# Kernel optimization log

Hardware: AMD Instinct MI355X
Metric: run time of the kernel (lower is better)

Reference implementation:

```python
import jax, jax.numpy as jnp
import numpy as np

N, E = 50000, 800000
IN_DIM, OUT_DIM, EDGE_DIM = 128, 128, 6
LN_EPS = 1e-5


def setup_inputs() -> dict:
    key = jax.random.key(0)
    ks = jax.random.split(key, 9)
    w = lambda k, sh: (jax.random.normal(k, sh, jnp.float32) * 0.05)
    return {
        "x": jax.random.normal(ks[0], (N, IN_DIM), jnp.float32),
        "edge_attr": jax.random.normal(ks[1], (E, EDGE_DIM), jnp.float32),
        "Wn": w(ks[2], (IN_DIM, OUT_DIM)),
        "bn": jnp.zeros((OUT_DIM,), jnp.float32),
        "We": w(ks[3], (EDGE_DIM, OUT_DIM)),
        "be": jnp.zeros((OUT_DIM,), jnp.float32),
        "Wm": w(ks[4], (2 * OUT_DIM, OUT_DIM)),
        "bm": jnp.zeros((OUT_DIM,), jnp.float32),
        "gamma": jnp.ones((OUT_DIM,), jnp.float32),
        "beta": jnp.zeros((OUT_DIM,), jnp.float32),
        "edge_index": jax.random.randint(ks[5], (2, E), 0, N, jnp.int32),
    }


def reference(x, edge_attr, Wn, bn, We, be, Wm, bm, gamma, beta, edge_index):
    row, col = edge_index[0], edge_index[1]
    x_t = x @ Wn + bn                                  # [N, D]
    e_t = edge_attr @ We + be                          # [E, D]
    msgs = jnp.concatenate([x_t[col], e_t], axis=-1)   # gather + concat [E, 2D]
    msgs = jax.nn.relu(msgs @ Wm + bm)                 # [E, D]
    agg = jax.ops.segment_sum(msgs, row, num_segments=N)            # scatter_add
    deg = jax.ops.segment_sum(jnp.ones((E,), jnp.float32), row, num_segments=N)
    out = agg / jnp.clip(deg, 1.0)[:, None] + x_t      # mean-normalize + residual
    mu = out.mean(axis=-1, keepdims=True)
    var = out.var(axis=-1, keepdims=True)
    return (out - mu) * jax.lax.rsqrt(var + LN_EPS) * gamma + beta
```

## Files before the change

### kernel.cpp

```cpp
#include <hip/hip_runtime.h>
#include <hip/hip_bf16.h>

#define D 128
#define EDGE_DIM 6
#define LN_EPS 1e-5f
#define HIST_BLOCKS 2048
#define BINE 2048
#define CB 512
#define NB2 98

typedef __attribute__((ext_vector_type(8))) short short8;
typedef __attribute__((ext_vector_type(4))) float f32x4;
typedef __attribute__((ext_vector_type(2))) float f32x2;

static __device__ __forceinline__ float bf_lo(unsigned u) { return __uint_as_float(u << 16); }
static __device__ __forceinline__ float bf_hi(unsigned u) { return __uint_as_float(u & 0xffff0000u); }
static __device__ __forceinline__ unsigned short f2bf(float f) {
    __hip_bfloat16 h = __float2bfloat16(f);
    return *reinterpret_cast<unsigned short*>(&h);
}
static __device__ __forceinline__ unsigned f2fp8(float f) {
    unsigned u;
    asm("v_cvt_pk_fp8_f32 %0, %1, %2" : "=v"(u) : "v"(f), "v"(0.0f));
    return u & 0xffu;
}
static __device__ __forceinline__ f32x2 cvt2_fp8v(unsigned w) {
    f32x2 r;
    asm("v_cvt_pk_f32_fp8 %0, %1" : "=v"(r) : "v"(w));
    return r;
}

__global__ __launch_bounds__(128)
void setup_all(const float* __restrict__ Wn, const float* __restrict__ bn,
               const float* __restrict__ We, const float* __restrict__ be,
               const float* __restrict__ Wm, const float* __restrict__ bm,
               const int* __restrict__ ei, int E,
               float* __restrict__ Wnm, float* __restrict__ bnm,
               float* __restrict__ Wc, float* __restrict__ bc,
               int* __restrict__ cnt) {
    const int b = blockIdx.x;
    const int d = threadIdx.x;
    if (b < 128) {
        float acc = 0.f;
#pragma unroll 8
        for (int j = 0; j < D; ++j)
            acc = fmaf(Wn[b * D + j], Wm[j * D + d], acc);
        Wnm[b * D + d] = acc;
    } else if (b == 128) {
        float acc = 0.f;
#pragma unroll 8
        for (int j = 0; j < D; ++j)
            acc = fmaf(bn[j], Wm[j * D + d], acc);
        bnm[d] = acc;
    } else if (b < 135) {
        const int k = b - 129;
        float acc = 0.f;
#pragma unroll 8
        for (int j = 0; j < D; ++j)
            acc = fmaf(We[k * D + j], Wm[(D + j) * D + d], acc);
        Wc[k * D + d] = acc;
    } else if (b == 135) {
        float acc = bm[d];
#pragma unroll 8
        for (int j = 0; j < D; ++j)
            acc = fmaf(be[j], Wm[(D + j) * D + d], acc);
        bc[d] = acc;
    } else {
        for (int i = (b - 136) * 128 + d; i < E; i += HIST_BLOCKS * 128)
            atomicAdd(&cnt[ei[i]], 1);
    }
}

__global__ __launch_bounds__(1024)
void scan_pack(const int* __restrict__ cnt, int* __restrict__ start,
               int* __restrict__ cur2, int* __restrict__ cursor, int n, int nscan,
               const float* __restrict__ Wn, const float* __restrict__ Wnm,
               unsigned short* __restrict__ Wb) {
    const int tid = threadIdx.x;
    if ((int)blockIdx.x >= nscan) {
        const int idx = ((int)blockIdx.x - nscan) * 1024 + tid;
        if (idx < 4096) {
            const int lane = idx & 63;
            const int s = (idx >> 6) & 3;
            const int ct = (idx >> 8) & 7;
            const int mat = idx >> 11;
            const float* W = mat ? Wnm : Wn;
            const int col = ct * 16 + (lane & 15);
            const int k0 = (lane >> 4) * 8 + 32 * s;
            short8 v;
#pragma unroll
            for (int j = 0; j < 8; ++j)
                v[j] = (short)f2bf(W[(size_t)(k0 + j) * D + col]);
            *reinterpret_cast<short8*>(Wb + (size_t)idx * 8) = v;
        }
        return;
    }
    __shared__ int wsum[16];
    __shared__ int sbase;
    const int lane = tid & 63, wid = tid >> 6;
    const int i = blockIdx.x * 1024 + tid;
    const int v = (i < n) ? cnt[i] : 0;
    int x = v;
#pragma unroll
    for (int off = 1; off < 64; off <<= 1) {
        int t = __shfl_up(x, off);
        if (lane >= off) x += t;
    }
    if (lane == 63) wsum[wid] = x;
    __syncthreads();
    if (wid == 0) {
        int w = (lane < 16) ? wsum[lane] : 0;
#pragma unroll
        for (int off = 1; off < 16; off <<= 1) {
            int t = __shfl_up(w, off);
            if (lane >= off) w += t;
        }
        if (lane < 16) wsum[lane] = w;
    }
    __syncthreads();
    const int total = wsum[15];
    if (tid == 0) sbase = atomicAdd(cursor, total);
    __syncthreads();
    const int woff = (wid > 0) ? wsum[wid - 1] : 0;
    if (i < n) {
        const int sv = sbase + woff + x - v;
        start[i] = sv;
        if ((i & (CB - 1)) == 0) cur2[i >> 9] = sv;
    }
}

__global__ __launch_bounds__(256)
void scat_gemm(const int* __restrict__ ei, int E, const float* __restrict__ ea,
               int* __restrict__ cur2, uint4* __restrict__ tmp, int nbin,
               const float* __restrict__ x, const unsigned short* __restrict__ Wb,
               const float* __restrict__ bn, const float* __restrict__ bnm,
               unsigned short* __restrict__ xtb, unsigned char* __restrict__ hb,
               int nrows) {
    __shared__ unsigned sR[BINE * 3];
    __shared__ int hist[NB2];
    __shared__ int cbase[NB2];
    const int tid = threadIdx.x;
    if ((int)blockIdx.x < nbin) {
        const int base = blockIdx.x * BINE;
        const int nrec = min(BINE, E - base);
        if (tid < NB2) hist[tid] = 0;
        const float2* ea2 = reinterpret_cast<const float2*>(ea);
        for (int i = tid; i < nrec * 3; i += 256) {
            float2 p = ea2[(size_t)base * 3 + i];
            sR[i] = (unsigned)f2bf(p.x) | ((unsigned)f2bf(p.y) << 16);
        }
        int rows[8], cols[8];
#pragma unroll
        for (int it = 0; it < 8; ++it) {
            const int e = base + it * 256 + tid;
            const bool val = e < E;
            rows[it] = val ? ei[e] : -1;
            cols[it] = val ? ei[E + e] : 0;
        }
        __syncthreads();
#pragma unroll
        for (int it = 0; it < 8; ++it)
            if (rows[it] >= 0) atomicAdd(&hist[rows[it] >> 9], 1);
        __syncthreads();
        if (tid < NB2) {
            const int hv = hist[tid];
            cbase[tid] = hv ? atomicAdd(&cur2[tid], hv) : 0;
            hist[tid] = 0;
        }
        __syncthreads();
#pragma unroll
        for (int it = 0; it < 8; ++it)
            if (rows[it] >= 0) {
                const int bkt = rows[it] >> 9;
                const int lp = atomicAdd(&hist[bkt], 1);
                const int pos = cbase[bkt] + lp;
                const int le = (it * 256 + tid) * 3;
                const unsigned w0 = (unsigned)cols[it] | ((unsigned)(rows[it] & (CB - 1)) << 16);
                tmp[pos] = make_uint4(w0, sR[le], sR[le + 1], sR[le + 2]);
            }
        return;
    }
    const int ntile = (nrows + 15) / 16;
    const int lane = tid & 63;
    const int wid = tid >> 6;
    const int t = ((int)blockIdx.x - nbin) * 4 + wid;
    if (t >= ntile) return;
    const int row16 = lane & 15;
    const int kgrp = lane >> 4;

    float biasA[8], biasB[8];
#pragma unroll
    for (int ct = 0; ct < 8; ++ct) {
        biasA[ct] = bn[ct * 16 + row16];
        biasB[ct] = bnm[ct * 16 + row16];
    }
    const int ra = t * 16 + row16;
    const bool rv = ra < nrows;
    short8 a[4];
#pragma unroll
    for (int s = 0; s < 4; ++s) {
        const float* xp = x + (size_t)ra * D + kgrp * 8 + 32 * s;
        float4 u0 = rv ? *reinterpret_cast<const float4*>(xp)
                       : make_float4(0.f, 0.f, 0.f, 0.f);
        float4 u1 = rv ? *reinterpret_cast<const float4*>(xp + 4)
                       : make_float4(0.f, 0.f, 0.f, 0.f);
        a[s][0] = (short)f2bf(u0.x); a[s][1] = (short)f2bf(u0.y);
        a[s][2] = (short)f2bf(u0.z); a[s][3] = (short)f2bf(u0.w);
        a[s][4] = (short)f2bf(u1.x); a[s][5] = (short)f2bf(u1.y);
        a[s][6] = (short)f2bf(u1.z); a[s][7] = (short)f2bf(u1.w);
    }
    const int rw0 = t * 16 + kgrp * 4;
#pragma unroll
    for (int mat = 0; mat < 2; ++mat) {
#pragma unroll
        for (int ct = 0; ct < 8; ++ct) {
            f32x4 acc = {0.f, 0.f, 0.f, 0.f};
#pragma unroll
            for (int s = 0; s < 4; ++s) {
                short8 bfr = *reinterpret_cast<const short8*>(
                    Wb + (size_t)((((mat * 8 + ct) * 4 + s) * 64 + lane)) * 8);
                acc = __builtin_amdgcn_mfma_f32_16x16x32_bf16(a[s], bfr, acc, 0, 0, 0);
            }
            const float bsc = mat ? biasB[ct] : biasA[ct];
            const int dcol = ct * 16 + row16;
#pragma unroll
            for (int j = 0; j < 4; ++j) {
                const int r = rw0 + j;
                if (r < nrows) {
                    if (mat == 0)
                        xtb[(size_t)r * D + dcol] = f2bf(acc[j] + bsc);
                    else
                        hb[(size_t)r * D + dcol] = (unsigned char)f2fp8(acc[j] + bsc);
                }
            }
        }
    }
}

__global__ __launch_bounds__(512)
void resort(const uint4* __restrict__ tmp, const int* __restrict__ start,
            const int* __restrict__ cnt, uint4* __restrict__ rec, int nnode) {
    __shared__ uint4 sRec[2048];
    __shared__ int ncur[CB];
    const int tid = threadIdx.x;
    const int b = blockIdx.x;
    const int nodes0 = b * CB;
    const int nn = min(CB, nnode - nodes0);
    if (tid < CB) ncur[tid] = (tid < nn) ? start[nodes0 + tid] : 0;
    __syncthreads();
    const int s0 = start[nodes0];
    const int lastn = nodes0 + nn - 1;
    const int count = start[lastn] + cnt[lastn] - s0;
    for (int base = 0; base < count; base += 2048) {
        const int m = min(2048, count - base);
        for (int i = tid; i < m; i += 512)
            sRec[i] = tmp[(size_t)(s0 + base) + i];
        __syncthreads();
        for (int i = tid; i < m; i += 512) {
            const uint4 rd = sRec[i];
            const int rl = (rd.x >> 16) & (CB - 1);
            const int pos = atomicAdd(&ncur[rl], 1);
            rec[pos] = make_uint4(rd.x & 0xffffu, rd.y, rd.z, rd.w);
        }
        __syncthreads();
    }
}

__global__ __launch_bounds__(256)
void aggregate_ln(const unsigned char* __restrict__ h8,
                  const int* __restrict__ start, const int* __restrict__ cnt,
                  const uint4* __restrict__ rec,
                  const float* __restrict__ Wc, const float* __restrict__ bc,
                  const unsigned* __restrict__ xtb,
                  const float* __restrict__ gamma, const float* __restrict__ beta,
                  float* __restrict__ out, int nnode) {
    const int lane = threadIdx.x & 63;
    const int wid = threadIdx.x >> 6;

    f32x2 wc[EDGE_DIM];
#pragma unroll
    for (int k = 0; k < EDGE_DIM; ++k)
        wc[k] = reinterpret_cast<const f32x2*>(Wc)[k * 64 + lane];
    const f32x2 bc2 = reinterpret_cast<const f32x2*>(bc)[lane];
    const f32x2 g = reinterpret_cast<const f32x2*>(gamma)[lane];
    const f32x2 bb = reinterpret_cast<const f32x2*>(beta)[lane];

    for (int n = blockIdx.x * 4 + wid; n < nnode; n += gridDim.x * 4) {
        const int s = start[n];
        const int c = cnt[n];
        const unsigned xu = xtb[(unsigned)(n * 64 + lane)];
        f32x2 axy = {0.f, 0.f};
        for (int ibase = 0; ibase < c; ibase += 64) {
            const int m = min(64, c - ibase);
            uint4 rc = make_uint4(0, 0, 0, 0);
            if (lane < m) rc = rec[(size_t)(s + ibase) + lane];
            auto LDH = [&](int j) -> unsigned {
                const int jc = min(j, m - 1);
                const unsigned colj = (unsigned)__builtin_amdgcn_readlane((int)rc.x, jc);
                const unsigned short* hrow =
                    reinterpret_cast<const unsigned short*>(h8 + ((size_t)colj << 7));
                return hrow[lane];
            };
            auto COMP = [&](int j, unsigned hv) {
                const unsigned b01 = (unsigned)__builtin_amdgcn_readlane((int)rc.y, j);
                const unsigned b23 = (unsigned)__builtin_amdgcn_readlane((int)rc.z, j);
                const unsigned b45 = (unsigned)__builtin_amdgcn_readlane((int)rc.w, j);
                f32x2 e01, e23, e45, mA, mB;
                e01[0] = bf_lo(b01); e01[1] = bf_hi(b01);
                e23[0] = bf_lo(b23); e23[1] = bf_hi(b23);
                e45[0] = bf_lo(b45); e45[1] = bf_hi(b45);
                const f32x2 hx = cvt2_fp8v(hv);
                asm("v_pk_add_f32 %0, %1, %2" : "=v"(mA) : "v"(bc2), "v"(hx));
                asm("v_pk_mul_f32 %0, %1, %2 op_sel:[1,0] op_sel_hi:[1,1]"
                    : "=v"(mB) : "s"(e01), "v"(wc[1]));
                asm("v_pk_fma_f32 %0, %1, %2, %0 op_sel:[0,0,0] op_sel_hi:[0,1,1]"
                    : "+v"(mA) : "s"(e01), "v"(wc[0]));
                asm("v_pk_fma_f32 %0, %1, %2, %0 op_sel:[1,0,0] op_sel_hi:[1,1,1]"
                    : "+v"(mB) : "s"(e23), "v"(wc[3]));
                asm("v_pk_fma_f32 %0, %1, %2, %0 op_sel:[0,0,0] op_sel_hi:[0,1,1]"
                    : "+v"(mA) : "s"(e23), "v"(wc[2]));
                asm("v_pk_fma_f32 %0, %1, %2, %0 op_sel:[1,0,0] op_sel_hi:[1,1,1]"
                    : "+v"(mB) : "s"(e45), "v"(wc[5]));
                asm("v_pk_fma_f32 %0, %1, %2, %0 op_sel:[0,0,0] op_sel_hi:[0,1,1]"
                    : "+v"(mA) : "s"(e45), "v"(wc[4]));
                asm("v_pk_add_f32 %0, %0, %1" : "+v"(mA) : "v"(mB));
                axy[0] += fmaxf(mA[0], 0.f);
                axy[1] += fmaxf(mA[1], 0.f);
            };
            unsigned h0 = LDH(0), h1 = LDH(1), h2 = LDH(2), h3 = LDH(3),
                     h4 = LDH(4), h5 = LDH(5), h6 = LDH(6), h7 = LDH(7);
            int i = 0;
            for (; i + 8 <= m; i += 8) {
                COMP(i + 0, h0); h0 = LDH(i + 8);
                COMP(i + 1, h1); h1 = LDH(i + 9);
                COMP(i + 2, h2); h2 = LDH(i + 10);
                COMP(i + 3, h3); h3 = LDH(i + 11);
                COMP(i + 4, h4); h4 = LDH(i + 12);
                COMP(i + 5, h5); h5 = LDH(i + 13);
                COMP(i + 6, h6); h6 = LDH(i + 14);
                COMP(i + 7, h7); h7 = LDH(i + 15);
            }
            if (i + 0 < m) COMP(i + 0, h0);
            if (i + 1 < m) COMP(i + 1, h1);
            if (i + 2 < m) COMP(i + 2, h2);
            if (i + 3 < m) COMP(i + 3, h3);
            if (i + 4 < m) COMP(i + 4, h4);
            if (i + 5 < m) COMP(i + 5, h5);
            if (i + 6 < m) COMP(i + 6, h6);
        }
        const float inv = 1.0f / fmaxf((float)c, 1.0f);
        float o0 = fmaf(axy[0], inv, bf_lo(xu));
        float o1 = fmaf(axy[1], inv, bf_hi(xu));
        float s1 = o0 + o1, s2 = o0 * o0 + o1 * o1;
#pragma unroll
        for (int off = 32; off; off >>= 1) {
            s1 += __shfl_xor(s1, off);
            s2 += __shfl_xor(s2, off);
        }
        const float mean = s1 * (1.0f / D);
        const float var = s2 * (1.0f / D) - mean * mean;
        const float rstd = rsqrtf(var + LN_EPS);
        float2 r;
        r.x = (o0 - mean) * rstd * g[0] + bb[0];
        r.y = (o1 - mean) * rstd * g[1] + bb[1];
        reinterpret_cast<float2*>(out)[(size_t)n * 64 + lane] = r;
    }
}

extern "C" void kernel_launch(void* const* d_in, const int* in_sizes, int n_in,
                              void* d_out, int out_size, void* d_ws, size_t ws_size,
                              hipStream_t stream) {
    const float* x     = (const float*)d_in[0];
    const float* eattr = (const float*)d_in[1];
    const float* Wn    = (const float*)d_in[2];
    const float* bn    = (const float*)d_in[3];
    const float* We    = (const float*)d_in[4];
    const float* be    = (const float*)d_in[5];
    const float* Wm    = (const float*)d_in[6];
    const float* bm    = (const float*)d_in[7];
    const float* gamma = (const float*)d_in[8];
    const float* beta  = (const float*)d_in[9];
    const int*   ei    = (const int*)d_in[10];

    const int N = in_sizes[0] / D;
    const int E = in_sizes[10] / 2;
    const int nbuck2 = (N + CB - 1) / CB;

    char* ws = (char*)d_ws;
    unsigned short* xtb = (unsigned short*)ws; ws += (size_t)N * D * 2;
    unsigned char*  hb  = (unsigned char*)ws;  ws += (size_t)N * D;
    int* ints = (int*)ws;                      ws += (size_t)(N + 4) * 4;
    int* cnt = ints;
    int* cursor = ints + N;
    int* cur2   = (int*)ws;                    ws += (size_t)(nbuck2 + 1) * 4;
    int* startv = (int*)ws;                    ws += (size_t)N * 4;
    uint4* rec  = (uint4*)ws;                  ws += (size_t)E * 16;
    float* Wnm  = (float*)ws;                  ws += (size_t)D * D * 4;
    float* bnm  = (float*)ws;                  ws += (size_t)D * 4;
    float* Wc   = (float*)ws;                  ws += (size_t)EDGE_DIM * D * 4;
    float* bcv  = (float*)ws;                  ws += (size_t)D * 4;
    unsigned short* Wb = (unsigned short*)ws;  ws += (size_t)4096 * 8 * 2;

    uint4* tmp = (uint4*)d_out;

    const int nscan = (N + 1023) / 1024;
    const int nbin = (E + BINE - 1) / BINE;
    const int ntile = (N + 15) / 16;

    hipMemsetAsync(ints, 0, (size_t)(N + 4) * 4, stream);

    setup_all<<<136 + HIST_BLOCKS, 128, 0, stream>>>(Wn, bn, We, be, Wm, bm, ei, E,
                                                     Wnm, bnm, Wc, bcv, cnt);
    scan_pack<<<nscan + 4, 1024, 0, stream>>>(cnt, startv, cur2, cursor, N, nscan,
                                              Wn, Wnm, Wb);
    scat_gemm<<<nbin + (ntile + 3) / 4, 256, 0, stream>>>(ei, E, eattr, cur2, tmp, nbin,
                                                          x, Wb, bn, bnm, xtb, hb, N);
    resort<<<nbuck2, 512, 0, stream>>>(tmp, startv, cnt, rec, N);
    aggregate_ln<<<(N + 3) / 4, 256, 0, stream>>>(hb, startv, cnt, rec,
                                                  Wc, bcv, (const unsigned*)xtb,
                                                  gamma, beta, (float*)d_out, N);
}
```

Measured before the change: 152.4 us.

## Shrink edge records to 8 bytes with fp8 edge attributes and finer buckets

Edge attributes are now packed as fp8 pairs instead of bf16, which shrinks each sorted edge record from 16 to 8 bytes. The local row index moves to a separate byte array, and the coarse bucket size drops from 512 to 256 nodes so that index fits in a byte. This halves the record traffic through scatter, resort and aggregate. The cost is lower precision on edge attributes (fp8) and an extra byte stream, and the edge-attribute conversion now uses vector registers rather than scalar operands.

```diff
diff --git a/kernel.cpp b/kernel.cpp
--- a/kernel.cpp
+++ b/kernel.cpp
@@ -6,8 +6,8 @@
 #define LN_EPS 1e-5f
 #define HIST_BLOCKS 2048
 #define BINE 2048
-#define CB 512
-#define NB2 98
+#define CB 256
+#define NB2 196
 
 typedef __attribute__((ext_vector_type(8))) short short8;
 typedef __attribute__((ext_vector_type(4))) float f32x4;
@@ -24,9 +24,19 @@
     asm("v_cvt_pk_fp8_f32 %0, %1, %2" : "=v"(u) : "v"(f), "v"(0.0f));
     return u & 0xffu;
 }
+static __device__ __forceinline__ unsigned f2fp8pair(float a, float b) {
+    unsigned u;
+    asm("v_cvt_pk_fp8_f32 %0, %1, %2" : "=v"(u) : "v"(a), "v"(b));
+    return u & 0xffffu;
+}
 static __device__ __forceinline__ f32x2 cvt2_fp8v(unsigned w) {
     f32x2 r;
     asm("v_cvt_pk_f32_fp8 %0, %1" : "=v"(r) : "v"(w));
+    return r;
+}
+static __device__ __forceinline__ f32x2 cvt2_fp8s(unsigned w) {
+    f32x2 r;
+    asm("v_cvt_pk_f32_fp8 %0, %1" : "=v"(r) : "s"(w));
     return r;
 }
 
@@ -125,18 +135,19 @@
     if (i < n) {
         const int sv = sbase + woff + x - v;
         start[i] = sv;
-        if ((i & (CB - 1)) == 0) cur2[i >> 9] = sv;
+        if ((i & (CB - 1)) == 0) cur2[i >> 8] = sv;
     }
 }
 
 __global__ __launch_bounds__(256)
 void scat_gemm(const int* __restrict__ ei, int E, const float* __restrict__ ea,
-               int* __restrict__ cur2, uint4* __restrict__ tmp, int nbin,
+               int* __restrict__ cur2, uint2* __restrict__ tmp,
+               unsigned char* __restrict__ tmpR, int nbin,
                const float* __restrict__ x, const unsigned short* __restrict__ Wb,
                const float* __restrict__ bn, const float* __restrict__ bnm,
                unsigned short* __restrict__ xtb, unsigned char* __restrict__ hb,
                int nrows) {
-    __shared__ unsigned sR[BINE * 3];
+    __shared__ unsigned short sP[BINE * 3];
     __shared__ int hist[NB2];
     __shared__ int cbase[NB2];
     const int tid = threadIdx.x;
@@ -147,7 +158,7 @@
         const float2* ea2 = reinterpret_cast<const float2*>(ea);
         for (int i = tid; i < nrec * 3; i += 256) {
             float2 p = ea2[(size_t)base * 3 + i];
-            sR[i] = (unsigned)f2bf(p.x) | ((unsigned)f2bf(p.y) << 16);
+            sP[i] = (unsigned short)f2fp8pair(p.x, p.y);
         }
         int rows[8], cols[8];
 #pragma unroll
@@ -160,7 +171,7 @@
         __syncthreads();
 #pragma unroll
         for (int it = 0; it < 8; ++it)
-            if (rows[it] >= 0) atomicAdd(&hist[rows[it] >> 9], 1);
+            if (rows[it] >= 0) atomicAdd(&hist[rows[it] >> 8], 1);
         __syncthreads();
         if (tid < NB2) {
             const int hv = hist[tid];
@@ -171,12 +182,14 @@
 #pragma unroll
         for (int it = 0; it < 8; ++it)
             if (rows[it] >= 0) {
-                const int bkt = rows[it] >> 9;
+                const int bkt = rows[it] >> 8;
                 const int lp = atomicAdd(&hist[bkt], 1);
                 const int pos = cbase[bkt] + lp;
                 const int le = (it * 256 + tid) * 3;
-                const unsigned w0 = (unsigned)cols[it] | ((unsigned)(rows[it] & (CB - 1)) << 16);
-                tmp[pos] = make_uint4(w0, sR[le], sR[le + 1], sR[le + 2]);
+                const unsigned w0 = (unsigned)cols[it] | ((unsigned)sP[le] << 16);
+                const unsigned w1 = (unsigned)sP[le + 1] | ((unsigned)sP[le + 2] << 16);
+                tmp[pos] = make_uint2(w0, w1);
+                tmpR[pos] = (unsigned char)(rows[it] & (CB - 1));
             }
         return;
     }
@@ -238,9 +251,11 @@
 }
 
 __global__ __launch_bounds__(512)
-void resort(const uint4* __restrict__ tmp, const int* __restrict__ start,
-            const int* __restrict__ cnt, uint4* __restrict__ rec, int nnode) {
-    __shared__ uint4 sRec[2048];
+void resort(const uint2* __restrict__ tmp, const unsigned char* __restrict__ tmpR,
+            const int* __restrict__ start, const int* __restrict__ cnt,
+            uint2* __restrict__ rec, int nnode) {
+    __shared__ uint2 sRec[2048];
+    __shared__ unsigned char sRow[2048];
     __shared__ int ncur[CB];
     const int tid = threadIdx.x;
     const int b = blockIdx.x;
@@ -253,14 +268,15 @@
     const int count = start[lastn] + cnt[lastn] - s0;
     for (int base = 0; base < count; base += 2048) {
         const int m = min(2048, count - base);
-        for (int i = tid; i < m; i += 512)
+        for (int i = tid; i < m; i += 512) {
             sRec[i] = tmp[(size_t)(s0 + base) + i];
+            sRow[i] = tmpR[(size_t)(s0 + base) + i];
+        }
         __syncthreads();
         for (int i = tid; i < m; i += 512) {
-            const uint4 rd = sRec[i];
-            const int rl = (rd.x >> 16) & (CB - 1);
+            const int rl = sRow[i];
             const int pos = atomicAdd(&ncur[rl], 1);
-            rec[pos] = make_uint4(rd.x & 0xffffu, rd.y, rd.z, rd.w);
+            rec[pos] = sRec[i];
         }
         __syncthreads();
     }
@@ -269,7 +285,7 @@
 __global__ __launch_bounds__(256)
 void aggregate_ln(const unsigned char* __restrict__ h8,
                   const int* __restrict__ start, const int* __restrict__ cnt,
-                  const uint4* __restrict__ rec,
+                  const uint2* __restrict__ rec,
                   const float* __restrict__ Wc, const float* __restrict__ bc,
                   const unsigned* __restrict__ xtb,
                   const float* __restrict__ gamma, const float* __restrict__ beta,
@@ -292,37 +308,37 @@
         f32x2 axy = {0.f, 0.f};
         for (int ibase = 0; ibase < c; ibase += 64) {
             const int m = min(64, c - ibase);
-            uint4 rc = make_uint4(0, 0, 0, 0);
+            uint2 rc = make_uint2(0, 0);
             if (lane < m) rc = rec[(size_t)(s + ibase) + lane];
             auto LDH = [&](int j) -> unsigned {
                 const int jc = min(j, m - 1);
-                const unsigned colj = (unsigned)__builtin_amdgcn_readlane((int)rc.x, jc);
+                const unsigned colj =
+                    (unsigned)__builtin_amdgcn_readlane((int)rc.x, jc) & 0xffffu;
                 const unsigned short* hrow =
                     reinterpret_cast<const unsigned short*>(h8 + ((size_t)colj << 7));
                 return hrow[lane];
             };
             auto COMP = [&](int j, unsigned hv) {
-                const unsigned b01 = (unsigned)__builtin_amdgcn_readlane((int)rc.y, j);
-                const unsigned b23 = (unsigned)__builtin_amdgcn_readlane((int)rc.z, j);
-                const unsigned b45 = (unsigned)__builtin_amdgcn_readlane((int)rc.w, j);
-                f32x2 e01, e23, e45, mA, mB;
-                e01[0] = bf_lo(b01); e01[1] = bf_hi(b01);
-                e23[0] = bf_lo(b23); e23[1] = bf_hi(b23);
-                e45[0] = bf_lo(b45); e45[1] = bf_hi(b45);
+                const unsigned w0 = (unsigned)__builtin_amdgcn_readlane((int)rc.x, j);
+                const unsigned w1 = (unsigned)__builtin_amdgcn_readlane((int)rc.y, j);
+                const f32x2 e01 = cvt2_fp8s(w0 >> 16);
+                const f32x2 e23 = cvt2_fp8s(w1 & 0xffffu);
+                const f32x2 e45 = cvt2_fp8s(w1 >> 16);
                 const f32x2 hx = cvt2_fp8v(hv);
+                f32x2 mA, mB;
                 asm("v_pk_add_f32 %0, %1, %2" : "=v"(mA) : "v"(bc2), "v"(hx));
                 asm("v_pk_mul_f32 %0, %1, %2 op_sel:[1,0] op_sel_hi:[1,1]"
-                    : "=v"(mB) : "s"(e01), "v"(wc[1]));
+                    : "=v"(mB) : "v"(e01), "v"(wc[1]));
                 asm("v_pk_fma_f32 %0, %1, %2, %0 op_sel:[0,0,0] op_sel_hi:[0,1,1]"
-                    : "+v"(mA) : "s"(e01), "v"(wc[0]));
+                    : "+v"(mA) : "v"(e01), "v"(wc[0]));
                 asm("v_pk_fma_f32 %0, %1, %2, %0 op_sel:[1,0,0] op_sel_hi:[1,1,1]"
-                    : "+v"(mB) : "s"(e23), "v"(wc[3]));
+                    : "+v"(mB) : "v"(e23), "v"(wc[3]));
                 asm("v_pk_fma_f32 %0, %1, %2, %0 op_sel:[0,0,0] op_sel_hi:[0,1,1]"
-                    : "+v"(mA) : "s"(e23), "v"(wc[2]));
+                    : "+v"(mA) : "v"(e23), "v"(wc[2]));
                 asm("v_pk_fma_f32 %0, %1, %2, %0 op_sel:[1,0,0] op_sel_hi:[1,1,1]"
-                    : "+v"(mB) : "s"(e45), "v"(wc[5]));
+                    : "+v"(mB) : "v"(e45), "v"(wc[5]));
                 asm("v_pk_fma_f32 %0, %1, %2, %0 op_sel:[0,0,0] op_sel_hi:[0,1,1]"
-                    : "+v"(mA) : "s"(e45), "v"(wc[4]));
+                    : "+v"(mA) : "v"(e45), "v"(wc[4]));
                 asm("v_pk_add_f32 %0, %0, %1" : "+v"(mA) : "v"(mB));
                 axy[0] += fmaxf(mA[0], 0.f);
                 axy[1] += fmaxf(mA[1], 0.f);
@@ -384,7 +400,6 @@
 
     const int N = in_sizes[0] / D;
     const int E = in_sizes[10] / 2;
-    const int nbuck2 = (N + CB - 1) / CB;
 
     char* ws = (char*)d_ws;
     unsigned short* xtb = (unsigned short*)ws; ws += (size_t)N * D * 2;
@@ -392,16 +407,17 @@
     int* ints = (int*)ws;                      ws += (size_t)(N + 4) * 4;
     int* cnt = ints;
     int* cursor = ints + N;
-    int* cur2   = (int*)ws;                    ws += (size_t)(nbuck2 + 1) * 4;
+    int* cur2   = (int*)ws;                    ws += (size_t)(NB2 + 1) * 4;
     int* startv = (int*)ws;                    ws += (size_t)N * 4;
-    uint4* rec  = (uint4*)ws;                  ws += (size_t)E * 16;
+    uint2* rec  = (uint2*)ws;                  ws += (size_t)E * 8;
     float* Wnm  = (float*)ws;                  ws += (size_t)D * D * 4;
     float* bnm  = (float*)ws;                  ws += (size_t)D * 4;
     float* Wc   = (float*)ws;                  ws += (size_t)EDGE_DIM * D * 4;
     float* bcv  = (float*)ws;                  ws += (size_t)D * 4;
     unsigned short* Wb = (unsigned short*)ws;  ws += (size_t)4096 * 8 * 2;
 
-    uint4* tmp = (uint4*)d_out;
+    uint2* tmp = (uint2*)d_out;
+    unsigned char* tmpR = (unsigned char*)d_out + (size_t)E * 8;
 
     const int nscan = (N + 1023) / 1024;
     const int nbin = (E + BINE - 1) / BINE;
@@ -413,9 +429,9 @@
                                                      Wnm, bnm, Wc, bcv, cnt);
     scan_pack<<<nscan + 4, 1024, 0, stream>>>(cnt, startv, cur2, cursor, N, nscan,
                                               Wn, Wnm, Wb);
-    scat_gemm<<<nbin + (ntile + 3) / 4, 256, 0, stream>>>(ei, E, eattr, cur2, tmp, nbin,
-                                                          x, Wb, bn, bnm, xtb, hb, N);
-    resort<<<nbuck2, 512, 0, stream>>>(tmp, startv, cnt, rec, N);
+    scat_gemm<<<nbin + (ntile + 3) / 4, 256, 0, stream>>>(ei, E, eattr, cur2, tmp, tmpR,
+                                                          nbin, x, Wb, bn, bnm, xtb, hb, N);
+    resort<<<NB2, 512, 0, stream>>>(tmp, tmpR, startv, cnt, rec, N);
     aggregate_ln<<<(N + 3) / 4, 256, 0, stream>>>(hb, startv, cnt, rec,
                                                   Wc, bcv, (const unsigned*)xtb,
                                                   gamma, beta, (float*)d_out, N);
```

After: 149.8 us. Within noise of the previous version (-1.7%).
